# Kernel optimization log

Hardware: AMD Instinct MI355X
Metric: run time of the kernel (lower is better)

The kernel has to match this reference:

```python
import jax, jax.numpy as jnp
import numpy as np
import math

EMBED_DIM = 1024
NUM_HEADS = 16
HEAD_DIM = EMBED_DIM // NUM_HEADS
BATCH = 2
SEQ = 2048


def setup_inputs() -> dict:
    key = jax.random.key(0)
    ks = jax.random.split(key, 9)
    s = 1.0 / math.sqrt(EMBED_DIM)
    return {
        "x": jax.random.normal(ks[0], (BATCH, SEQ, EMBED_DIM), jnp.float32),
        "Wq": jax.random.normal(ks[1], (EMBED_DIM, EMBED_DIM), jnp.float32) * s,
        "bq": jnp.zeros((EMBED_DIM,), jnp.float32),
        "Wk": jax.random.normal(ks[2], (EMBED_DIM, EMBED_DIM), jnp.float32) * s,
        "bk": jnp.zeros((EMBED_DIM,), jnp.float32),
        "Wv": jax.random.normal(ks[3], (EMBED_DIM, EMBED_DIM), jnp.float32) * s,
        "bv": jnp.zeros((EMBED_DIM,), jnp.float32),
        "Wo": jax.random.normal(ks[4], (EMBED_DIM, EMBED_DIM), jnp.float32) * s,
        "bo": jnp.zeros((EMBED_DIM,), jnp.float32),
    }


def _rope_tables(seq_len, dim, dtype):
    inv_freq = 1.0 / (10000.0 ** (jnp.arange(0, dim, 2, dtype=jnp.float32) / dim))
    t = jnp.arange(seq_len, dtype=jnp.float32)
    freqs = jnp.einsum("i,j->ij", t, inv_freq)          # [S, D/2]
    emb = jnp.concatenate([freqs, freqs], axis=-1)       # [S, D]
    return jnp.cos(emb).astype(dtype), jnp.sin(emb).astype(dtype)


def _rotate_half(x):
    x1, x2 = jnp.split(x, 2, axis=-1)
    return jnp.concatenate([-x2, x1], axis=-1)


def _apply_rope(x, cos, sin):
    # x: [B, S, H, D]; cos/sin: [S, D] -> broadcast over batch & heads
    cos = cos[None, :, None, :]
    sin = sin[None, :, None, :]
    return x * cos + _rotate_half(x) * sin


def reference(x, Wq, bq, Wk, bk, Wv, bv, Wo, bo):
    B, S, E = x.shape
    H, D = NUM_HEADS, HEAD_DIM
    q = (x @ Wq + bq).reshape(B, S, H, D)
    k = (x @ Wk + bk).reshape(B, S, H, D)
    v = (x @ Wv + bv).reshape(B, S, H, D)
    cos, sin = _rope_tables(S, D, x.dtype)
    q = _apply_rope(q, cos, sin)
    k = _apply_rope(k, cos, sin)
    scale = 1.0 / math.sqrt(D)
    # scores: [B, H, S, S]
    scores = jnp.einsum("bqhd,bkhd->bhqk", q, k) * scale
    attn = jax.nn.softmax(scores, axis=-1)
    ctx = jnp.einsum("bhqk,bkhd->bqhd", attn, v).reshape(B, S, E)
    return ctx @ Wo + bo
```

## Files before the change

### kernel.cpp

```cpp
#include <hip/hip_runtime.h>
#include <math.h>

#define B_ 2
#define S_ 2048
#define E_ 1024
#define H_ 16
#define D_ 64
#define M_ (B_*S_)

typedef _Float16 f16x8 __attribute__((ext_vector_type(8)));
typedef __fp16   h16x2 __attribute__((ext_vector_type(2)));
typedef float    f32x4 __attribute__((ext_vector_type(4)));

__device__ __forceinline__ ushort f2h(float f) {
    _Float16 h = (_Float16)f;
    return __builtin_bit_cast(ushort, h);
}

__device__ __forceinline__ void gload_lds16(const ushort* g, ushort* l) {
    __builtin_amdgcn_global_load_lds(
        (const __attribute__((address_space(1))) unsigned int*)g,
        (__attribute__((address_space(3))) unsigned int*)l, 16, 0, 0);
}

__global__ void prep_kernel(const float* __restrict__ x,
                            const float* __restrict__ W0, const float* __restrict__ W1,
                            const float* __restrict__ W2, const float* __restrict__ W3,
                            ushort* __restrict__ xf, ushort* __restrict__ WT,
                            float* __restrict__ ct, float* __restrict__ st)
{
    const int bid = blockIdx.x;
    const int tid = threadIdx.x;
    __shared__ float tile[32][33];

    if (bid < 4096) {
        const int z = bid >> 10, rem = bid & 1023;
        const int k0 = (rem >> 5) * 32, nb = (rem & 31) * 32;
        const float* W = (z == 0) ? W0 : (z == 1) ? W1 : (z == 2) ? W2 : W3;
        const size_t zoff = (size_t)z * E_ * E_;
        const int tx = tid & 31, ty = tid >> 5;
        #pragma unroll
        for (int i = 0; i < 4; i++) {
            int r = i * 8 + ty;
            tile[r][tx] = W[(size_t)(k0 + r) * E_ + nb + tx];
        }
        __syncthreads();
        #pragma unroll
        for (int i = 0; i < 4; i++) {
            int r = i * 8 + ty;
            WT[zoff + (size_t)(nb + r) * E_ + k0 + tx] = f2h(tile[tx][r]);
        }
    } else if (bid < 8192) {
        const int i = (bid - 4096) * 1024 + tid * 4;
        float4 v = *(const float4*)&x[i];
        *(ushort4*)&xf[i] = make_ushort4(f2h(v.x), f2h(v.y), f2h(v.z), f2h(v.w));
    } else {
        const int i = (bid - 8192) * 256 + tid;
        const int j = i & 31, pos = i >> 5;
        float invf = (float)pow(10000.0, -(double)j / 32.0);
        float ang  = (float)pos * invf;
        ct[i] = (float)cos((double)ang);
        st[i] = (float)sin((double)ang);
    }
}

#define GBM 128
#define GBN 128
#define GBK 32

__global__ __launch_bounds__(256, 3)
void gemm_f16(const ushort* __restrict__ A, const ushort* __restrict__ WTp,
              const float* __restrict__ b0, const float* __restrict__ b1,
              const float* __restrict__ b2,
              const float* __restrict__ ct, const float* __restrict__ st,
              ushort* __restrict__ outQ, ushort* __restrict__ outK,
              ushort* __restrict__ outV, float* __restrict__ outF,
              int force_mode)
{
    __shared__ __align__(16) ushort lA[GBM * GBK];
    __shared__ __align__(16) ushort lB[GBN * GBK];

    const int tid  = threadIdx.x;
    const int wv   = tid >> 6, lane = tid & 63;
    const int c    = lane & 15, qd = lane >> 4;
    const int rh   = wv >> 1, chn = wv & 1;

    const int mode = (force_mode >= 0) ? force_mode : (int)blockIdx.z;
    const size_t zoff = (force_mode >= 0) ? 0 : (size_t)blockIdx.z * (E_ * E_);
    const ushort* Bt = WTp + zoff;

    const int m0 = blockIdx.y * GBM, n0 = blockIdx.x * GBN;

    const ushort* gsrc = (wv < 2) ? A : Bt;
    ushort* ldst = (wv < 2) ? lA : lB;
    const int rowbase = ((wv < 2) ? m0 : n0) + (wv & 1) * 64;
    const int lofs = (wv & 1) * 64 * GBK;
    const int srow = lane >> 2;
    const int soct = (lane & 3) * 8;

    f32x4 acc[4][4] = {};

    for (int k0i = 0; k0i < E_; k0i += GBK) {
        #pragma unroll
        for (int cc = 0; cc < 4; cc++) {
            const ushort* g = gsrc + (size_t)(rowbase + cc * 16 + srow) * E_ + k0i + soct;
            gload_lds16(g, ldst + lofs + cc * 512);
        }
        __syncthreads();

        f16x8 af[4], bf[4];
        #pragma unroll
        for (int mt = 0; mt < 4; mt++)
            af[mt] = *(const f16x8*)&lA[(rh * 64 + mt * 16 + c) * GBK + qd * 8];
        #pragma unroll
        for (int nt = 0; nt < 4; nt++)
            bf[nt] = *(const f16x8*)&lB[(chn * 64 + nt * 16 + c) * GBK + qd * 8];
        #pragma unroll
        for (int mt = 0; mt < 4; mt++)
            #pragma unroll
            for (int nt = 0; nt < 4; nt++)
                acc[mt][nt] = __builtin_amdgcn_mfma_f32_16x16x32_f16(af[mt], bf[nt], acc[mt][nt], 0, 0, 0);
        __syncthreads();
    }

    const float* bias = (mode == 0) ? b0 : (mode == 1) ? b1 : (mode == 2) ? b2 : b0;
    const int colbase = n0 + chn * 64;

    if (mode == 3) {
        #pragma unroll
        for (int mt = 0; mt < 4; mt++)
            #pragma unroll
            for (int r = 0; r < 4; r++) {
                const int row = m0 + rh * 64 + mt * 16 + qd * 4 + r;
                #pragma unroll
                for (int nt = 0; nt < 4; nt++) {
                    const int col = colbase + nt * 16 + c;
                    outF[(size_t)row * E_ + col] = acc[mt][nt][r] + bias[col];
                }
            }
    } else if (mode == 2) {
        const int hd = colbase >> 6;
        #pragma unroll
        for (int mt = 0; mt < 4; mt++)
            #pragma unroll
            for (int r = 0; r < 4; r++) {
                const int row = m0 + rh * 64 + mt * 16 + qd * 4 + r;
                const int bb = row >> 11, sl = row & (S_ - 1);
                const size_t base = ((size_t)(bb * H_ + hd) * (S_ / 8) + (sl >> 3)) * 512 + (sl & 7);
                #pragma unroll
                for (int nt = 0; nt < 4; nt++) {
                    const int d = nt * 16 + c;
                    outV[base + (size_t)d * 8] = f2h(acc[mt][nt][r] + bias[colbase + d]);
                }
            }
    } else {
        ushort* O = (mode == 0) ? outQ : outK;
        const float sc = (mode == 0) ? 0.125f : 1.0f;
        #pragma unroll
        for (int mt = 0; mt < 4; mt++)
            #pragma unroll
            for (int r = 0; r < 4; r++) {
                const int row = m0 + rh * 64 + mt * 16 + qd * 4 + r;
                const int pos = row & (S_ - 1);
                #pragma unroll
                for (int p = 0; p < 2; p++) {
                    const int j32 = p * 16 + c;
                    const float cth = ct[pos * 32 + j32], sth = st[pos * 32 + j32];
                    const float v1 = acc[mt][p][r]     + bias[colbase + p * 16 + c];
                    const float v2 = acc[mt][p + 2][r] + bias[colbase + (p + 2) * 16 + c];
                    O[(size_t)row * E_ + colbase + p * 16 + c]       = f2h((v1 * cth - v2 * sth) * sc);
                    O[(size_t)row * E_ + colbase + (p + 2) * 16 + c] = f2h((v2 * cth + v1 * sth) * sc);
                }
            }
    }
}

#define PST 80

__global__ __launch_bounds__(256, 6)
void attn_mfma(const ushort* __restrict__ Qf, const ushort* __restrict__ Kf,
               const ushort* __restrict__ Vf, ushort* __restrict__ ctxf)
{
    __shared__ ushort Kls[64 * PST];
    __shared__ ushort Vls[8 * 520];

    const int tid  = threadIdx.x;
    const int wv   = tid >> 6;
    const int lane = tid & 63;
    const int c    = lane & 15;
    const int qd   = lane >> 4;

    const int ntq = S_ / 64;
    const int bh  = blockIdx.x / ntq;
    const int qt  = blockIdx.x % ntq;
    const int b   = bh >> 4, h = bh & 15;
    const int q0  = qt * 64;

    const size_t qbase = ((size_t)b * S_ + q0) * E_ + h * 64;
    const size_t kbase = (size_t)b * S_ * E_ + h * 64;
    const size_t vbase = (size_t)bh * S_ * 64;

    const int r0 = tid >> 3,         dc0 = (tid & 7) * 8;
    const int r1 = (tid + 256) >> 3, dc1 = dc0;
    const int e0 = tid * 8,          e1 = (tid + 256) * 8;

    *(uint4*)&Kls[r0 * PST + dc0] = *(const uint4*)&Qf[qbase + (size_t)r0 * E_ + dc0];
    *(uint4*)&Kls[r1 * PST + dc1] = *(const uint4*)&Qf[qbase + (size_t)r1 * E_ + dc1];
    __syncthreads();
    f16x8 qfrag[2];
    {
        const int qrow = wv * 16 + c;
        #pragma unroll
        for (int kc = 0; kc < 2; kc++)
            qfrag[kc] = *(const f16x8*)&Kls[qrow * PST + kc * 32 + qd * 8];
    }
    __syncthreads();

    f32x4 acc[4] = {};
    float lsum = 0.0f;

    uint4 kpre0 = *(const uint4*)&Kf[kbase + (size_t)r0 * E_ + dc0];
    uint4 kpre1 = *(const uint4*)&Kf[kbase + (size_t)r1 * E_ + dc1];
    uint4 vpre0 = *(const uint4*)&Vf[vbase + e0];
    uint4 vpre1 = *(const uint4*)&Vf[vbase + e1];

    const int srcA = c + ((qd & 1) << 5);
    const int srcB = srcA + 16;
    const bool hi = qd >= 2;

    for (int k0 = 0; k0 < S_; k0 += 64) {
        *(uint4*)&Kls[r0 * PST + dc0] = kpre0;
        *(uint4*)&Kls[r1 * PST + dc1] = kpre1;
        *(uint4*)&Vls[(e0 >> 9) * 520 + (e0 & 511)] = vpre0;
        *(uint4*)&Vls[(e1 >> 9) * 520 + (e1 & 511)] = vpre1;
        __syncthreads();

        if (k0 + 64 < S_) {
            kpre0 = *(const uint4*)&Kf[kbase + (size_t)(k0 + 64 + r0) * E_ + dc0];
            kpre1 = *(const uint4*)&Kf[kbase + (size_t)(k0 + 64 + r1) * E_ + dc1];
            vpre0 = *(const uint4*)&Vf[vbase + (size_t)(k0 + 64) * 64 + e0];
            vpre1 = *(const uint4*)&Vf[vbase + (size_t)(k0 + 64) * 64 + e1];
        }

        f32x4 sv[4];
        #pragma unroll
        for (int t = 0; t < 4; t++) {
            f32x4 s = {};
            #pragma unroll
            for (int kc = 0; kc < 2; kc++) {
                f16x8 kf = *(const f16x8*)&Kls[(t * 16 + c) * PST + kc * 32 + qd * 8];
                s = __builtin_amdgcn_mfma_f32_16x16x32_f16(kf, qfrag[kc], s, 0, 0, 0);
            }
            sv[t] = s;
        }
        #pragma unroll
        for (int t = 0; t < 4; t++)
            #pragma unroll
            for (int r = 0; r < 4; r++) {
                const float p = __expf(sv[t][r]);
                sv[t][r] = p;
                lsum += p;
            }

        unsigned int pk0[4], pk1[4];
        #pragma unroll
        for (int t = 0; t < 4; t++) {
            h16x2 a   = __builtin_amdgcn_cvt_pkrtz(sv[t][0], sv[t][1]);
            h16x2 bb2 = __builtin_amdgcn_cvt_pkrtz(sv[t][2], sv[t][3]);
            pk0[t] = __builtin_bit_cast(unsigned int, a);
            pk1[t] = __builtin_bit_cast(unsigned int, bb2);
        }

        f16x8 pfrag[2];
        #pragma unroll
        for (int kc = 0; kc < 2; kc++) {
            const int t0 = kc * 2, t1 = kc * 2 + 1;
            unsigned int s00 = (unsigned int)__shfl((int)pk0[t0], srcA);
            unsigned int s01 = (unsigned int)__shfl((int)pk0[t1], srcA);
            unsigned int s10 = (unsigned int)__shfl((int)pk1[t0], srcA);
            unsigned int s11 = (unsigned int)__shfl((int)pk1[t1], srcA);
            unsigned int s20 = (unsigned int)__shfl((int)pk0[t0], srcB);
            unsigned int s21 = (unsigned int)__shfl((int)pk0[t1], srcB);
            unsigned int s30 = (unsigned int)__shfl((int)pk1[t0], srcB);
            unsigned int s31 = (unsigned int)__shfl((int)pk1[t1], srcB);
            uint4 pd;
            pd.x = hi ? s01 : s00;
            pd.y = hi ? s11 : s10;
            pd.z = hi ? s21 : s20;
            pd.w = hi ? s31 : s30;
            pfrag[kc] = __builtin_bit_cast(f16x8, pd);
        }

        #pragma unroll
        for (int dt = 0; dt < 4; dt++) {
            #pragma unroll
            for (int kc = 0; kc < 2; kc++) {
                const int kg = kc * 4 + qd;
                f16x8 vfr = *(const f16x8*)&Vls[kg * 520 + (dt * 16 + c) * 8];
                acc[dt] = __builtin_amdgcn_mfma_f32_16x16x32_f16(vfr, pfrag[kc], acc[dt], 0, 0, 0);
            }
        }
        __syncthreads();
    }

    float l = lsum;
    l += __shfl_xor(l, 16);
    l += __shfl_xor(l, 32);
    const float inv = 1.0f / l;

    const size_t orow = ((size_t)b * S_ + q0 + wv * 16 + c) * E_ + h * 64;
    #pragma unroll
    for (int dt = 0; dt < 4; dt++) {
        ushort4 o = make_ushort4(f2h(acc[dt][0] * inv), f2h(acc[dt][1] * inv),
                                 f2h(acc[dt][2] * inv), f2h(acc[dt][3] * inv));
        *(ushort4*)&ctxf[orow + dt * 16 + qd * 4] = o;
    }
}

extern "C" void kernel_launch(void* const* d_in, const int* in_sizes, int n_in,
                              void* d_out, int out_size, void* d_ws, size_t ws_size,
                              hipStream_t stream)
{
    const float* x  = (const float*)d_in[0];
    const float* Wq = (const float*)d_in[1];
    const float* bq = (const float*)d_in[2];
    const float* Wk = (const float*)d_in[3];
    const float* bk = (const float*)d_in[4];
    const float* Wv = (const float*)d_in[5];
    const float* bv = (const float*)d_in[6];
    const float* Wo = (const float*)d_in[7];
    const float* bo = (const float*)d_in[8];
    float* out = (float*)d_out;

    ushort* Qb = (ushort*)d_ws;
    ushort* Kb = Qb + (size_t)M_ * E_;
    ushort* Vf = Kb + (size_t)M_ * E_;
    ushort* xf = Vf + (size_t)M_ * E_;
    ushort* WT = xf + (size_t)M_ * E_;
    float*  ct = (float*)(WT + (size_t)4 * E_ * E_);
    float*  st = ct + S_ * 32;
    ushort* ctxf = Qb;

    hipLaunchKernelGGL(prep_kernel, dim3(8448), dim3(256), 0, stream,
                       x, Wq, Wk, Wv, Wo, xf, WT, ct, st);

    hipLaunchKernelGGL(gemm_f16, dim3(E_ / GBN, M_ / GBM, 3), dim3(256), 0, stream,
                       xf, WT, bq, bk, bv, ct, st,
                       Qb, Kb, Vf, (float*)nullptr, -1);

    hipLaunchKernelGGL(attn_mfma, dim3(B_ * H_ * (S_ / 64)), dim3(256), 0, stream,
                       Qb, Kb, Vf, ctxf);

    hipLaunchKernelGGL(gemm_f16, dim3(E_ / GBN, M_ / GBM, 1), dim3(256), 0, stream,
                       ctxf, WT + (size_t)3 * E_ * E_, bo, bo, bo, ct, st,
                       (ushort*)nullptr, (ushort*)nullptr, (ushort*)nullptr, out, 3);
}
```

Before: 216.5 us.

## Restructure attention with 128-key tiles, split-K across waves, swizzled LDS and direct loads

The attention kernel now stages 128-key K/V tiles into swizzled LDS through direct global-to-LDS loads. Each wave handles all 64 queries over a 32-key slice, and partial outputs and row sums are reduced across waves through LDS at the end. The projection epilogue writes Q/K with an XOR swizzle and V in a transposed, swizzled tile layout to match. This removes the cross-lane shuffle repacking of P, cuts LDS bank conflicts and raises MFMA work per load, at the cost of more registers (launch bounds drop to 3 blocks), an end-of-kernel reduction, and loss of the register prefetch overlap.

```diff
diff --git a/kernel.cpp b/kernel.cpp
--- a/kernel.cpp
+++ b/kernel.cpp
@@ -8,9 +8,10 @@
 #define D_ 64
 #define M_ (B_*S_)
 
-typedef _Float16 f16x8 __attribute__((ext_vector_type(8)));
-typedef __fp16   h16x2 __attribute__((ext_vector_type(2)));
-typedef float    f32x4 __attribute__((ext_vector_type(4)));
+typedef _Float16 f16x8  __attribute__((ext_vector_type(8)));
+typedef _Float16 f16x4v __attribute__((ext_vector_type(4)));
+typedef __fp16   h16x2  __attribute__((ext_vector_type(2)));
+typedef float    f32x4  __attribute__((ext_vector_type(4)));
 
 __device__ __forceinline__ ushort f2h(float f) {
     _Float16 h = (_Float16)f;
@@ -146,11 +147,14 @@
             for (int r = 0; r < 4; r++) {
                 const int row = m0 + rh * 64 + mt * 16 + qd * 4 + r;
                 const int bb = row >> 11, sl = row & (S_ - 1);
-                const size_t base = ((size_t)(bb * H_ + hd) * (S_ / 8) + (sl >> 3)) * 512 + (sl & 7);
+                const int tt = sl >> 7, key = sl & 127;
+                const int c4 = key >> 2, inner = key & 3;
+                const size_t base = (size_t)(bb * H_ + hd) * (S_ * D_) + tt * 8192;
                 #pragma unroll
                 for (int nt = 0; nt < 4; nt++) {
                     const int d = nt * 16 + c;
-                    outV[base + (size_t)d * 8] = f2h(acc[mt][nt][r] + bias[colbase + d]);
+                    outV[base + d * 128 + ((c4 ^ (d & 7)) * 4) + inner]
+                        = f2h(acc[mt][nt][r] + bias[colbase + d]);
                 }
             }
     } else {
@@ -162,158 +166,175 @@
             for (int r = 0; r < 4; r++) {
                 const int row = m0 + rh * 64 + mt * 16 + qd * 4 + r;
                 const int pos = row & (S_ - 1);
+                const int sw = row & 7;
                 #pragma unroll
                 for (int p = 0; p < 2; p++) {
                     const int j32 = p * 16 + c;
                     const float cth = ct[pos * 32 + j32], sth = st[pos * 32 + j32];
                     const float v1 = acc[mt][p][r]     + bias[colbase + p * 16 + c];
                     const float v2 = acc[mt][p + 2][r] + bias[colbase + (p + 2) * 16 + c];
-                    O[(size_t)row * E_ + colbase + p * 16 + c]       = f2h((v1 * cth - v2 * sth) * sc);
-                    O[(size_t)row * E_ + colbase + (p + 2) * 16 + c] = f2h((v2 * cth + v1 * sth) * sc);
+                    const float o1 = (v1 * cth - v2 * sth) * sc;
+                    const float o2 = (v2 * cth + v1 * sth) * sc;
+                    const int cd1 = p * 16 + c, cd2 = cd1 + 32;
+                    O[(size_t)row * E_ + colbase + (((cd1 >> 3) ^ sw) * 8) + (cd1 & 7)] = f2h(o1);
+                    O[(size_t)row * E_ + colbase + (((cd2 >> 3) ^ sw) * 8) + (cd2 & 7)] = f2h(o2);
                 }
             }
     }
 }
 
-#define PST 80
-
-__global__ __launch_bounds__(256, 6)
+__global__ __launch_bounds__(256, 3)
 void attn_mfma(const ushort* __restrict__ Qf, const ushort* __restrict__ Kf,
-               const ushort* __restrict__ Vf, ushort* __restrict__ ctxf)
+               const ushort* __restrict__ Vfg, ushort* __restrict__ ctxf)
 {
-    __shared__ ushort Kls[64 * PST];
-    __shared__ ushort Vls[8 * 520];
-
-    const int tid  = threadIdx.x;
-    const int wv   = tid >> 6;
-    const int lane = tid & 63;
-    const int c    = lane & 15;
-    const int qd   = lane >> 4;
-
-    const int ntq = S_ / 64;
-    const int bh  = blockIdx.x / ntq;
-    const int qt  = blockIdx.x % ntq;
-    const int b   = bh >> 4, h = bh & 15;
-    const int q0  = qt * 64;
-
-    const size_t qbase = ((size_t)b * S_ + q0) * E_ + h * 64;
-    const size_t kbase = (size_t)b * S_ * E_ + h * 64;
-    const size_t vbase = (size_t)bh * S_ * 64;
-
-    const int r0 = tid >> 3,         dc0 = (tid & 7) * 8;
-    const int r1 = (tid + 256) >> 3, dc1 = dc0;
-    const int e0 = tid * 8,          e1 = (tid + 256) * 8;
-
-    *(uint4*)&Kls[r0 * PST + dc0] = *(const uint4*)&Qf[qbase + (size_t)r0 * E_ + dc0];
-    *(uint4*)&Kls[r1 * PST + dc1] = *(const uint4*)&Qf[qbase + (size_t)r1 * E_ + dc1];
+    __shared__ __align__(16) ushort Kls[128 * 64];
+    __shared__ __align__(16) ushort Vls[64 * 128];
+
+    const int tid = threadIdx.x;
+    const int wv = tid >> 6, lane = tid & 63;
+    const int c = lane & 15, qd = lane >> 4;
+    const int cs = c & 7;
+
+    const int xcd = blockIdx.x & 7, ii = blockIdx.x >> 3;
+    const int bh = xcd * 4 + (ii & 3);
+    const int qtb = ii >> 2;
+    const int b = bh >> 4, h = bh & 15;
+    const int q0 = qtb * 64;
+
+    const size_t qrow0 = (size_t)b * S_ + q0;
+    const size_t krow0 = (size_t)b * S_;
+    const size_t vbase = (size_t)bh * (S_ * D_);
+
+    const int l8 = lane >> 3, l7 = lane & 7;
+    const int l16 = lane >> 4, l15 = lane & 15;
+
+    #pragma unroll
+    for (int j = 0; j < 2; j++) {
+        const int row = wv * 16 + j * 8 + l8;
+        const ushort* g = Qf + (qrow0 + row) * E_ + h * 64 + l7 * 8;
+        gload_lds16(g, Kls + wv * 1024 + j * 512);
+    }
     __syncthreads();
-    f16x8 qfrag[2];
-    {
-        const int qrow = wv * 16 + c;
+    f16x8 qfrag[4][2];
+    #pragma unroll
+    for (int qt = 0; qt < 4; qt++)
         #pragma unroll
         for (int kc = 0; kc < 2; kc++)
-            qfrag[kc] = *(const f16x8*)&Kls[qrow * PST + kc * 32 + qd * 8];
-    }
+            qfrag[qt][kc] = *(const f16x8*)&Kls[(qt * 16 + c) * 64 + (((kc * 4 + qd) ^ cs) * 8)];
     __syncthreads();
 
-    f32x4 acc[4] = {};
-    float lsum = 0.0f;
-
-    uint4 kpre0 = *(const uint4*)&Kf[kbase + (size_t)r0 * E_ + dc0];
-    uint4 kpre1 = *(const uint4*)&Kf[kbase + (size_t)r1 * E_ + dc1];
-    uint4 vpre0 = *(const uint4*)&Vf[vbase + e0];
-    uint4 vpre1 = *(const uint4*)&Vf[vbase + e1];
-
-    const int srcA = c + ((qd & 1) << 5);
-    const int srcB = srcA + 16;
-    const bool hi = qd >= 2;
-
-    for (int k0 = 0; k0 < S_; k0 += 64) {
-        *(uint4*)&Kls[r0 * PST + dc0] = kpre0;
-        *(uint4*)&Kls[r1 * PST + dc1] = kpre1;
-        *(uint4*)&Vls[(e0 >> 9) * 520 + (e0 & 511)] = vpre0;
-        *(uint4*)&Vls[(e1 >> 9) * 520 + (e1 & 511)] = vpre1;
-        __syncthreads();
-
-        if (k0 + 64 < S_) {
-            kpre0 = *(const uint4*)&Kf[kbase + (size_t)(k0 + 64 + r0) * E_ + dc0];
-            kpre1 = *(const uint4*)&Kf[kbase + (size_t)(k0 + 64 + r1) * E_ + dc1];
-            vpre0 = *(const uint4*)&Vf[vbase + (size_t)(k0 + 64) * 64 + e0];
-            vpre1 = *(const uint4*)&Vf[vbase + (size_t)(k0 + 64) * 64 + e1];
-        }
-
-        f32x4 sv[4];
-        #pragma unroll
-        for (int t = 0; t < 4; t++) {
-            f32x4 s = {};
-            #pragma unroll
-            for (int kc = 0; kc < 2; kc++) {
-                f16x8 kf = *(const f16x8*)&Kls[(t * 16 + c) * PST + kc * 32 + qd * 8];
-                s = __builtin_amdgcn_mfma_f32_16x16x32_f16(kf, qfrag[kc], s, 0, 0, 0);
-            }
-            sv[t] = s;
-        }
-        #pragma unroll
-        for (int t = 0; t < 4; t++)
-            #pragma unroll
-            for (int r = 0; r < 4; r++) {
-                const float p = __expf(sv[t][r]);
-                sv[t][r] = p;
-                lsum += p;
-            }
-
-        unsigned int pk0[4], pk1[4];
-        #pragma unroll
-        for (int t = 0; t < 4; t++) {
-            h16x2 a   = __builtin_amdgcn_cvt_pkrtz(sv[t][0], sv[t][1]);
-            h16x2 bb2 = __builtin_amdgcn_cvt_pkrtz(sv[t][2], sv[t][3]);
-            pk0[t] = __builtin_bit_cast(unsigned int, a);
-            pk1[t] = __builtin_bit_cast(unsigned int, bb2);
-        }
-
-        f16x8 pfrag[2];
-        #pragma unroll
-        for (int kc = 0; kc < 2; kc++) {
-            const int t0 = kc * 2, t1 = kc * 2 + 1;
-            unsigned int s00 = (unsigned int)__shfl((int)pk0[t0], srcA);
-            unsigned int s01 = (unsigned int)__shfl((int)pk0[t1], srcA);
-            unsigned int s10 = (unsigned int)__shfl((int)pk1[t0], srcA);
-            unsigned int s11 = (unsigned int)__shfl((int)pk1[t1], srcA);
-            unsigned int s20 = (unsigned int)__shfl((int)pk0[t0], srcB);
-            unsigned int s21 = (unsigned int)__shfl((int)pk0[t1], srcB);
-            unsigned int s30 = (unsigned int)__shfl((int)pk1[t0], srcB);
-            unsigned int s31 = (unsigned int)__shfl((int)pk1[t1], srcB);
-            uint4 pd;
-            pd.x = hi ? s01 : s00;
-            pd.y = hi ? s11 : s10;
-            pd.z = hi ? s21 : s20;
-            pd.w = hi ? s31 : s30;
-            pfrag[kc] = __builtin_bit_cast(f16x8, pd);
+    f32x4 acc[4][4] = {};
+    float lsum[4] = {0.f, 0.f, 0.f, 0.f};
+
+    #pragma unroll 1
+    for (int t = 0; t < 16; t++) {
+        const int k0 = t * 128;
+        if (wv < 2) {
+            #pragma unroll
+            for (int j = 0; j < 8; j++) {
+                const int row = wv * 64 + j * 8 + l8;
+                const ushort* g = Kf + (krow0 + k0 + row) * E_ + h * 64 + l7 * 8;
+                gload_lds16(g, Kls + wv * 4096 + j * 512);
+            }
+        } else {
+            #pragma unroll
+            for (int j = 0; j < 8; j++) {
+                const int drow = (wv - 2) * 32 + j * 4 + l16;
+                const ushort* g = Vfg + vbase + t * 8192 + drow * 128 + l15 * 8;
+                gload_lds16(g, Vls + (wv - 2) * 4096 + j * 512);
+            }
+        }
+        __syncthreads();
+
+        f16x4v bfrag[2][4];
+        #pragma unroll
+        for (int kt = 0; kt < 2; kt++) {
+            f16x8 kfr[2];
+            #pragma unroll
+            for (int kc = 0; kc < 2; kc++)
+                kfr[kc] = *(const f16x8*)&Kls[(wv * 32 + kt * 16 + c) * 64 + (((kc * 4 + qd) ^ cs) * 8)];
+            #pragma unroll
+            for (int qt = 0; qt < 4; qt++) {
+                f32x4 s = {};
+                s = __builtin_amdgcn_mfma_f32_16x16x32_f16(kfr[0], qfrag[qt][0], s, 0, 0, 0);
+                s = __builtin_amdgcn_mfma_f32_16x16x32_f16(kfr[1], qfrag[qt][1], s, 0, 0, 0);
+                const float p0 = __expf(s[0]), p1 = __expf(s[1]);
+                const float p2 = __expf(s[2]), p3 = __expf(s[3]);
+                lsum[qt] += (p0 + p1) + (p2 + p3);
+                h16x2 lo = __builtin_amdgcn_cvt_pkrtz(p0, p1);
+                h16x2 hi = __builtin_amdgcn_cvt_pkrtz(p2, p3);
+                uint2 u;
+                u.x = __builtin_bit_cast(unsigned int, lo);
+                u.y = __builtin_bit_cast(unsigned int, hi);
+                bfrag[kt][qt] = __builtin_bit_cast(f16x4v, u);
+            }
         }
 
         #pragma unroll
         for (int dt = 0; dt < 4; dt++) {
             #pragma unroll
-            for (int kc = 0; kc < 2; kc++) {
-                const int kg = kc * 4 + qd;
-                f16x8 vfr = *(const f16x8*)&Vls[kg * 520 + (dt * 16 + c) * 8];
-                acc[dt] = __builtin_amdgcn_mfma_f32_16x16x32_f16(vfr, pfrag[kc], acc[dt], 0, 0, 0);
-            }
-        }
-        __syncthreads();
-    }
-
-    float l = lsum;
-    l += __shfl_xor(l, 16);
-    l += __shfl_xor(l, 32);
-    const float inv = 1.0f / l;
-
-    const size_t orow = ((size_t)b * S_ + q0 + wv * 16 + c) * E_ + h * 64;
-    #pragma unroll
-    for (int dt = 0; dt < 4; dt++) {
-        ushort4 o = make_ushort4(f2h(acc[dt][0] * inv), f2h(acc[dt][1] * inv),
-                                 f2h(acc[dt][2] * inv), f2h(acc[dt][3] * inv));
-        *(ushort4*)&ctxf[orow + dt * 16 + qd * 4] = o;
+            for (int kt = 0; kt < 2; kt++) {
+                f16x4v vfr = *(const f16x4v*)&Vls[(dt * 16 + c) * 128 + (((wv * 8 + kt * 4 + qd) ^ cs) * 4)];
+                #pragma unroll
+                for (int qt = 0; qt < 4; qt++)
+                    acc[dt][qt] = __builtin_amdgcn_mfma_f32_16x16x16f16(vfr, bfrag[kt][qt], acc[dt][qt], 0, 0, 0);
+            }
+        }
+        __syncthreads();
+    }
+
+    float* red = (float*)Kls;
+    float* lsr = (float*)Vls;
+
+    #pragma unroll
+    for (int qt = 0; qt < 4; qt++) {
+        float v = lsum[qt];
+        v += __shfl_xor(v, 16);
+        v += __shfl_xor(v, 32);
+        lsum[qt] = v;
+    }
+    if (lane < 16) {
+        #pragma unroll
+        for (int qt = 0; qt < 4; qt++) lsr[wv * 64 + qt * 16 + lane] = lsum[qt];
+    }
+
+    f32x4 own[4];
+    #pragma unroll
+    for (int qt = 0; qt < 4; qt++)
+        own[qt] = (wv == 0) ? acc[0][qt] : (wv == 1) ? acc[1][qt]
+                : (wv == 2) ? acc[2][qt] : acc[3][qt];
+
+    #pragma unroll
+    for (int r = 1; r < 4; r++) {
+        const int ds = (wv + r) & 3;
+        #pragma unroll
+        for (int qt = 0; qt < 4; qt++) {
+            f32x4 sv = (ds == 0) ? acc[0][qt] : (ds == 1) ? acc[1][qt]
+                     : (ds == 2) ? acc[2][qt] : acc[3][qt];
+            *(f32x4*)&red[ds * 1024 + qt * 256 + lane * 4] = sv;
+        }
+        __syncthreads();
+        #pragma unroll
+        for (int qt = 0; qt < 4; qt++)
+            own[qt] += *(const f32x4*)&red[wv * 1024 + qt * 256 + lane * 4];
+        if (r < 3) __syncthreads();
+    }
+
+    float inv[4];
+    #pragma unroll
+    for (int qt = 0; qt < 4; qt++) {
+        const int q = qt * 16 + c;
+        inv[qt] = 1.0f / (lsr[q] + lsr[64 + q] + lsr[128 + q] + lsr[192 + q]);
+    }
+
+    const size_t obase = qrow0 * E_ + h * 64 + wv * 16 + qd * 4;
+    #pragma unroll
+    for (int qt = 0; qt < 4; qt++) {
+        f32x4 v = own[qt];
+        const float iq = inv[qt];
+        ushort4 o = make_ushort4(f2h(v[0] * iq), f2h(v[1] * iq),
+                                 f2h(v[2] * iq), f2h(v[3] * iq));
+        *(ushort4*)&ctxf[obase + (size_t)(qt * 16 + c) * E_] = o;
     }
 }
 
```

Result: faster. 210.9 us (-2.6%).
